# Performance work log

Hardware: AMD Instinct MI355X
Metric: run time of the kernel (lower is better)

The kernel has to match this reference:

```python
import jax, jax.numpy as jnp
import numpy as np

B, L, D = 2, 2048, 1024
H = 16          # num_heads == num_key_value_heads
FD = 16         # feature_dim (q/k head dim)
HD = D // H     # head_dim = 64 (v head dim)
EPS = 1e-5


def setup_inputs() -> dict:
    key = jax.random.key(0)
    k0, k1, k2, k3, k4 = jax.random.split(key, 5)
    scale = 0.02
    return {
        "hidden_states": jax.random.normal(k0, (B, L, D), jnp.float32),
        "Wq": jax.random.normal(k1, (D, H * FD), jnp.float32) * scale,
        "Wk": jax.random.normal(k2, (D, H * FD), jnp.float32) * scale,
        "Wv": jax.random.normal(k3, (D, H * HD), jnp.float32) * scale,
        "Wo": jax.random.normal(k4, (H * HD, D), jnp.float32) * scale,
    }


def reference(hidden_states, Wq, Wk, Wv, Wo):
    # projections (bias-free), split heads: b l (h d) -> b h l d
    q = (hidden_states @ Wq).reshape(B, L, H, FD).transpose(0, 2, 1, 3)
    k = (hidden_states @ Wk).reshape(B, L, H, FD).transpose(0, 2, 1, 3)
    v = (hidden_states @ Wv).reshape(B, L, H, HD).transpose(0, 2, 1, 3)

    # parallel_rebased: squared-dot-product kernel attention, causal,
    # row-normalized by the kernel sum (use_scale=True, use_normalize=True)
    qk_scale = FD ** -0.5
    s = jnp.einsum('bhqd,bhkd->bhqk', q * qk_scale, k)
    s = s * s  # quadratic feature map: (q.k)^2
    causal = jnp.tril(jnp.ones((L, L), dtype=bool))
    s = jnp.where(causal, s, 0.0)
    z = jnp.sum(s, axis=-1)  # [B,H,L]
    o = jnp.einsum('bhqk,bhkd->bhqd', s, v) / (z[..., None] + EPS)

    # merge heads: b h l d -> b l (h d), output projection
    o = o.transpose(0, 2, 1, 3).reshape(B, L, H * HD)
    return o @ Wo
```

## Files before the change

### kernel.cpp

```cpp
#include <hip/hip_runtime.h>
#include <hip/hip_bf16.h>

#define BB 2
#define LL 2048
#define DD 1024
#define HH 16
#define FD 16
#define HD 64
#define EPS 1e-5f
#define RQKV 1536
#define NFIX 4

typedef __attribute__((ext_vector_type(4))) float f32x4;
typedef __attribute__((ext_vector_type(8))) _Float16 f16x8;
typedef __attribute__((ext_vector_type(4))) _Float16 f16x4;

__global__ __launch_bounds__(256) void prep(
    const float* __restrict__ Wq, const float* __restrict__ Wk,
    const float* __restrict__ Wv, const float* __restrict__ Wo,
    const float* __restrict__ hs, _Float16* __restrict__ WqkvT,
    _Float16* __restrict__ WoT, float* __restrict__ QKVe,
    _Float16* __restrict__ HS16) {
  __shared__ __attribute__((aligned(16))) char smem[40960];
  const int bx = blockIdx.x;
  const int tid = threadIdx.x;

  if (bx >= 2608) {
    int idx = ((bx - 2608) * 256 + tid) * 16;
#pragma unroll
    for (int half = 0; half < 2; half++) {
      float4 a = *(const float4*)(hs + idx + half * 8);
      float4 b = *(const float4*)(hs + idx + half * 8 + 4);
      f16x8 p = {(_Float16)a.x, (_Float16)a.y, (_Float16)a.z, (_Float16)a.w,
                 (_Float16)b.x, (_Float16)b.y, (_Float16)b.z, (_Float16)b.w};
      *(f16x8*)(HS16 + idx + half * 8) = p;
    }
    return;
  }

  if (bx < 2560) {
    _Float16(*s)[40] = (_Float16(*)[40])smem;
    const float* src;
    _Float16* dst;
    int n0, ncol, drow, k0;
    if (bx < 1536) {
      int ct = bx % 48, kt = bx / 48;
      if (ct < 8) { src = Wq; n0 = ct * 32; ncol = 256; drow = n0; }
      else if (ct < 16) { src = Wk; n0 = (ct - 8) * 32; ncol = 256; drow = 256 + n0; }
      else { src = Wv; n0 = (ct - 16) * 32; ncol = 1024; drow = 512 + n0; }
      k0 = kt * 32;
      dst = WqkvT;
    } else {
      int i2 = bx - 1536;
      n0 = (i2 & 31) * 32; k0 = (i2 >> 5) * 32;
      src = Wo; ncol = DD; drow = n0; dst = WoT;
    }
    {
      int r = tid >> 3, c = (tid & 7) * 4;
      float4 v = *(const float4*)(src + (size_t)(k0 + r) * ncol + n0 + c);
      f16x4 p = {(_Float16)v.x, (_Float16)v.y, (_Float16)v.z, (_Float16)v.w};
      *(f16x4*)&s[r][c] = p;
    }
    __syncthreads();
    {
      int n = tid >> 3, kk = (tid & 7) * 4;
      f16x4 o = {s[kk + 0][n], s[kk + 1][n], s[kk + 2][n], s[kk + 3][n]};
      *(f16x4*)(dst + (size_t)(drow + n) * DD + k0 + kk) = o;
    }
    return;
  }

  float(*sHS)[DD] = (float(*)[DD])smem;
  float(*part)[8][32] = (float(*)[8][32])(smem + 32768);
  const int kg = tid >> 5, c = tid & 31;
  const int c0 = (bx - 2560) * 32;

  for (int i = tid; i < 8 * (DD / 4); i += 256) {
    int e = i / (DD / 4), col4 = (i % (DD / 4)) * 4;
    int b = e >> 2, r = e & 3;
    *(float4*)&sHS[e][col4] =
        *(const float4*)(hs + (size_t)(b * LL + r) * DD + col4);
  }
  __syncthreads();

  const float* W;
  int col, ncol;
  if (c0 < 256) { W = Wq; col = c0 + c; ncol = 256; }
  else if (c0 < 512) { W = Wk; col = (c0 - 256) + c; ncol = 256; }
  else { W = Wv; col = (c0 - 512) + c; ncol = 1024; }

  float acc[8] = {};
  const int d0 = kg * 128;
#pragma unroll 4
  for (int d = d0; d < d0 + 128; d++) {
    float wv = W[(size_t)d * ncol + col];
#pragma unroll
    for (int e = 0; e < 8; e++) acc[e] += sHS[e][d] * wv;
  }
#pragma unroll
  for (int e = 0; e < 8; e++) part[kg][e][c] = acc[e];
  __syncthreads();

  {
    int e = tid >> 5;
    float t = 0.f;
#pragma unroll
    for (int g = 0; g < 8; g++) t += part[g][e][c];
    QKVe[(size_t)e * RQKV + c0 + c] = t;
  }
}

template <typename OutT>
__global__ __launch_bounds__(256) void gemm_f16(
    const _Float16* __restrict__ A, const _Float16* __restrict__ Bt,
    OutT* __restrict__ C, int M, int N, int K) {
  __shared__ __attribute__((aligned(16))) _Float16 sA[128 * 64];
  __shared__ __attribute__((aligned(16))) _Float16 sB[64 * 64];
  const int tid = threadIdx.x;
  const int m0 = blockIdx.y * 128, n0 = blockIdx.x * 64;
  const int w = tid >> 6, lane = tid & 63, quad = lane >> 4, l16 = lane & 15;
  const int wm = (w >> 1) * 64, wn = (w & 1) * 32;

  const int sr = tid >> 1, p = tid & 1;
  const int brow = (tid & 127) >> 1;
  const _Float16* Ag = A + (size_t)(m0 + sr) * K + p * 32;
  const _Float16* Bg = Bt + (size_t)(n0 + brow) * K + p * 32;
  _Float16* sAw = &sA[sr * 64];
  _Float16* sBw = &sB[brow * 64];
  const int aswz = sr & 7, bswz = brow & 7;

  f32x4 acc[4][2];
#pragma unroll
  for (int i = 0; i < 4; i++)
#pragma unroll
    for (int j = 0; j < 2; j++) acc[i][j] = (f32x4){0.f, 0.f, 0.f, 0.f};

  f16x8 ar[4], br[4];
  auto LOAD = [&](int k0) {
#pragma unroll
    for (int i = 0; i < 4; i++) ar[i] = *(const f16x8*)(Ag + k0 + i * 8);
    if (tid < 128) {
#pragma unroll
      for (int i = 0; i < 4; i++) br[i] = *(const f16x8*)(Bg + k0 + i * 8);
    }
  };
  LOAD(0);

  for (int k0 = 0; k0 < K; k0 += 64) {
    __syncthreads();
#pragma unroll
    for (int i = 0; i < 4; i++)
      *(f16x8*)(sAw + (((4 * p + i) ^ aswz) * 8)) = ar[i];
    if (tid < 128) {
#pragma unroll
      for (int i = 0; i < 4; i++)
        *(f16x8*)(sBw + (((4 * p + i) ^ bswz) * 8)) = br[i];
    }
    __syncthreads();
    if (k0 + 64 < K) LOAD(k0 + 64);

#pragma unroll
    for (int s = 0; s < 2; s++) {
      f16x8 af[4], bf[2];
#pragma unroll
      for (int i = 0; i < 4; i++) {
        int row = wm + i * 16 + l16;
        int col = ((s * 4 + quad) ^ (row & 7)) * 8;
        af[i] = *(const f16x8*)&sA[row * 64 + col];
      }
#pragma unroll
      for (int j = 0; j < 2; j++) {
        int row = wn + j * 16 + l16;
        int col = ((s * 4 + quad) ^ (row & 7)) * 8;
        bf[j] = *(const f16x8*)&sB[row * 64 + col];
      }
#pragma unroll
      for (int i = 0; i < 4; i++)
#pragma unroll
        for (int j = 0; j < 2; j++)
          acc[i][j] = __builtin_amdgcn_mfma_f32_16x16x32_f16(af[i], bf[j], acc[i][j], 0, 0, 0);
    }
  }

#pragma unroll
  for (int i = 0; i < 4; i++)
#pragma unroll
    for (int j = 0; j < 2; j++)
#pragma unroll
      for (int r = 0; r < 4; r++) {
        const int row = m0 + wm + i * 16 + quad * 4 + r;
        const int col = n0 + wn + j * 16 + l16;
        C[(size_t)row * N + col] = (OutT)acc[i][j][r];
      }
}

#define SK5 24
#define SV5 136
#define SS5 88

__global__ __launch_bounds__(256, 4) void attn_mfma5(
    const _Float16* __restrict__ QKV, _Float16* __restrict__ O) {
  __shared__ __attribute__((aligned(16))) _Float16 sK[128 * SK5];
  __shared__ __attribute__((aligned(16))) _Float16 sVt[80 * SV5];
  __shared__ __attribute__((aligned(16))) _Float16 sS2[4 * 16 * SS5];

  const int bh = blockIdx.x;
  const int b = bh >> 4, h = bh & 15;
  const int qt = 31 - blockIdx.y;
  const int tid = threadIdx.x;
  const int w = tid >> 6;
  const int lane = tid & 63;
  const int quad = lane >> 4;
  const int l16 = lane & 15;
  const int gq = qt * 64 + w * 16;

  f16x8 qfrag = {};
  if (quad < 2) {
    qfrag = *(const f16x8*)(QKV +
        (size_t)(b * LL + gq + l16) * RQKV + h * FD + quad * 8);
    const _Float16 RT2 = (_Float16)1.41421356f;
#pragma unroll
    for (int i = 0; i < 8; i++) qfrag[i] = qfrag[i] * RT2;
  }

  for (int t = tid; t < 16 * SV5; t += 256) {
    int r = t / SV5, c = t % SV5;
    sVt[64 * SV5 + t] = (_Float16)((r == 0 && c < 128) ? 1.0f : 0.0f);
  }
  __syncthreads();
  const f16x8 zf0 = *(const f16x8*)&sVt[(64 + l16) * SV5 + quad * 8];
  const f16x8 zf1 = *(const f16x8*)&sVt[(64 + l16) * SV5 + 32 + quad * 8];

  f32x4 oacc[4];
  f32x4 zacc = (f32x4){0.f, 0.f, 0.f, 0.f};
#pragma unroll
  for (int nt = 0; nt < 4; nt++) oacc[nt] = (f32x4){0.f, 0.f, 0.f, 0.f};

  _Float16* sS2w = sS2 + w * 16 * SS5;

  const int nst = qt + 1;
  const int nkt = (nst + 1) >> 1;

  const int krow = tid >> 1, kcol = (tid & 1) * 8;
  f16x8 kreg;
  f16x8 vreg0, vreg1, vreg2, vreg3;
  auto LOAD = [&](int kt) {
    kreg = *(const f16x8*)(QKV +
        (size_t)(b * LL + kt * 128 + krow) * RQKV + 256 + h * FD + kcol);
    const _Float16* vp = QKV +
        (size_t)(b * LL + kt * 128 + lane) * RQKV + 512 + h * HD + w * 16;
    vreg0 = *(const f16x8*)vp;
    vreg1 = *(const f16x8*)(vp + 8);
    vp += (size_t)64 * RQKV;
    vreg2 = *(const f16x8*)vp;
    vreg3 = *(const f16x8*)(vp + 8);
  };
  LOAD(0);

  for (int kt = 0; kt < nkt; kt++) {
    __syncthreads();
    *(f16x8*)&sK[krow * SK5 + kcol] = kreg;
#pragma unroll
    for (int t = 0; t < 8; t++) sVt[(w * 16 + t) * SV5 + lane] = vreg0[t];
#pragma unroll
    for (int t = 0; t < 8; t++) sVt[(w * 16 + 8 + t) * SV5 + lane] = vreg1[t];
#pragma unroll
    for (int t = 0; t < 8; t++) sVt[(w * 16 + t) * SV5 + 64 + lane] = vreg2[t];
#pragma unroll
    for (int t = 0; t < 8; t++) sVt[(w * 16 + 8 + t) * SV5 + 64 + lane] = vreg3[t];
    __syncthreads();
    if (kt + 1 < nkt) LOAD(kt + 1);

#pragma unroll
    for (int hf = 0; hf < 2; hf++) {
      const int st = 2 * kt + hf;
      if (st >= nst) break;
      const int k0 = st * 64;
      const bool mask = (st == qt);

      f16x8 kf[4];
#pragma unroll
      for (int nt = 0; nt < 4; nt++) {
        f16x8 f = {};
        if (quad < 2)
          f = *(const f16x8*)&sK[(hf * 64 + nt * 16 + l16) * SK5 + quad * 8];
        kf[nt] = f;
      }

#pragma unroll
      for (int nt = 0; nt < 4; nt++) {
        f32x4 s = __builtin_amdgcn_mfma_f32_16x16x32_f16(
            qfrag, kf[nt], (f32x4){0.f, 0.f, 0.f, 0.f}, 0, 0, 0);
        const int gk = k0 + nt * 16 + l16;
#pragma unroll
        for (int r = 0; r < 4; r++) {
          float sv = s[r] * s[r];
          if (mask) sv = (gk <= gq + quad * 4 + r) ? sv : 0.0f;
          sS2w[(quad * 4 + r) * SS5 + nt * 16 + l16] = (_Float16)sv;
        }
      }
      __asm__ volatile("s_waitcnt lgkmcnt(0)" ::: "memory");

      f16x8 af0 = *(const f16x8*)&sS2w[l16 * SS5 + quad * 8];
      f16x8 af1 = *(const f16x8*)&sS2w[l16 * SS5 + 32 + quad * 8];

#pragma unroll
      for (int nt = 0; nt < 4; nt++) {
        f16x8 vf0 = *(const f16x8*)&sVt[(nt * 16 + l16) * SV5 + hf * 64 + quad * 8];
        f16x8 vf1 = *(const f16x8*)&sVt[(nt * 16 + l16) * SV5 + hf * 64 + 32 + quad * 8];
        oacc[nt] = __builtin_amdgcn_mfma_f32_16x16x32_f16(af0, vf0, oacc[nt], 0, 0, 0);
        oacc[nt] = __builtin_amdgcn_mfma_f32_16x16x32_f16(af1, vf1, oacc[nt], 0, 0, 0);
      }
      zacc = __builtin_amdgcn_mfma_f32_16x16x32_f16(af0, zf0, zacc, 0, 0, 0);
      zacc = __builtin_amdgcn_mfma_f32_16x16x32_f16(af1, zf1, zacc, 0, 0, 0);
    }
  }

  {
    float rz[4];
#pragma unroll
    for (int r = 0; r < 4; r++) {
      float zz = __shfl(zacc[r], lane & 48);
      rz[r] = 1.0f / (zz + 32.0f * EPS);
    }
#pragma unroll
    for (int nt = 0; nt < 4; nt++)
#pragma unroll
      for (int r = 0; r < 4; r++) {
        const int gqr = gq + quad * 4 + r;
        O[(size_t)(b * LL + gqr) * (HH * HD) + h * HD + nt * 16 + l16] =
            (_Float16)(oacc[nt][r] * rz[r]);
      }
  }
}

__global__ __launch_bounds__(256) void fix_final(
    const float* __restrict__ QKVe, _Float16* __restrict__ Oatt) {
  const int b = blockIdx.x >> 4, h = blockIdx.x & 15;
  const int tid = threadIdx.x;
  const int p = tid >> 6, d = tid & 63;

  float num = 0.f, z = 0.f;
  const float* qrow = QKVe + (size_t)(b * 4 + p) * RQKV + h * FD;
  for (int j = 0; j <= p; j++) {
    const float* krow = QKVe + (size_t)(b * 4 + j) * RQKV + 256 + h * FD;
    float s = 0.f;
#pragma unroll
    for (int f = 0; f < FD; f++) s += qrow[f] * krow[f];
    s *= 0.25f;
    s = s * s;
    z += s;
    num += s * QKVe[(size_t)(b * 4 + j) * RQKV + 512 + h * HD + d];
  }
  Oatt[(size_t)(b * LL + p) * (HH * HD) + h * HD + d] =
      (_Float16)(num / (z + EPS));
}

extern "C" void kernel_launch(void* const* d_in, const int* in_sizes, int n_in,
                              void* d_out, int out_size, void* d_ws, size_t ws_size,
                              hipStream_t stream) {
  const float* hs = (const float*)d_in[0];
  const float* Wq = (const float*)d_in[1];
  const float* Wk = (const float*)d_in[2];
  const float* Wv = (const float*)d_in[3];
  const float* Wo = (const float*)d_in[4];
  float* out = (float*)d_out;

  char* ws = (char*)d_ws;
  _Float16* WqkvT = (_Float16*)ws;
  _Float16* WoT   = (_Float16*)(ws + (3ull << 20));
  _Float16* HS16  = (_Float16*)(ws + (5ull << 20));
  _Float16* QKV   = (_Float16*)(ws + (13ull << 20));
  _Float16* Oatt  = (_Float16*)(ws + (25ull << 20));
  float*    QKVe  = (float*)(ws + (33ull << 20));

  const int M = BB * LL;

  prep<<<dim3(3632), 256, 0, stream>>>(Wq, Wk, Wv, Wo, hs, WqkvT, WoT, QKVe, HS16);

  gemm_f16<_Float16><<<dim3(RQKV / 64, M / 128), 256, 0, stream>>>(
      HS16, WqkvT, QKV, M, RQKV, DD);

  attn_mfma5<<<dim3(BB * HH, LL / 64), 256, 0, stream>>>(QKV, Oatt);

  fix_final<<<dim3(BB * HH), 256, 0, stream>>>(QKVe, Oatt);

  gemm_f16<float><<<dim3(DD / 64, M / 128), 256, 0, stream>>>(
      Oatt, WoT, out, M, DD, DD);
}
```

Before: 172.9 us.

## Keep squared scores in registers via transposed MFMA and permuted V layout

Computes the score tile as K·Qᵀ so each lane's accumulator lanes already match the A-operand layout of the next MFMA. The squared, masked scores are packed into f16 registers directly instead of round-tripping through a per-wave shared-memory buffer. To make this work, the V transpose in shared memory is stored with a permuted key-column index that matches the new score register ordering. Removing the scratch buffer frees LDS, and the launch-bounds occupancy hint rises from 4 to 5 blocks, at the cost of a more intricate lane-permutation invariant.

```diff
diff --git a/kernel.cpp b/kernel.cpp
--- a/kernel.cpp
+++ b/kernel.cpp
@@ -14,6 +14,7 @@
 typedef __attribute__((ext_vector_type(4))) float f32x4;
 typedef __attribute__((ext_vector_type(8))) _Float16 f16x8;
 typedef __attribute__((ext_vector_type(4))) _Float16 f16x4;
+typedef __attribute__((ext_vector_type(4))) unsigned int u32x4;
 
 __global__ __launch_bounds__(256) void prep(
     const float* __restrict__ Wq, const float* __restrict__ Wk,
@@ -194,15 +195,19 @@
       }
 }
 
+__device__ __forceinline__ unsigned pack_f16x2(float a, float b) {
+  unsigned short ua = __builtin_bit_cast(unsigned short, (_Float16)a);
+  unsigned short ub = __builtin_bit_cast(unsigned short, (_Float16)b);
+  return (unsigned)ua | ((unsigned)ub << 16);
+}
+
 #define SK5 24
 #define SV5 136
-#define SS5 88
-
-__global__ __launch_bounds__(256, 4) void attn_mfma5(
+
+__global__ __launch_bounds__(256, 5) void attn_mfma7(
     const _Float16* __restrict__ QKV, _Float16* __restrict__ O) {
   __shared__ __attribute__((aligned(16))) _Float16 sK[128 * SK5];
   __shared__ __attribute__((aligned(16))) _Float16 sVt[80 * SV5];
-  __shared__ __attribute__((aligned(16))) _Float16 sS2[4 * 16 * SS5];
 
   const int bh = blockIdx.x;
   const int b = bh >> 4, h = bh & 15;
@@ -214,6 +219,8 @@
   const int l16 = lane & 15;
   const int gq = qt * 64 + w * 16;
 
+  const int pc = (lane & 32) | ((lane & 12) << 1) | ((lane & 16) >> 2) | (lane & 3);
+
   f16x8 qfrag = {};
   if (quad < 2) {
     qfrag = *(const f16x8*)(QKV +
@@ -235,8 +242,6 @@
   f32x4 zacc = (f32x4){0.f, 0.f, 0.f, 0.f};
 #pragma unroll
   for (int nt = 0; nt < 4; nt++) oacc[nt] = (f32x4){0.f, 0.f, 0.f, 0.f};
-
-  _Float16* sS2w = sS2 + w * 16 * SS5;
 
   const int nst = qt + 1;
   const int nkt = (nst + 1) >> 1;
@@ -261,13 +266,13 @@
     __syncthreads();
     *(f16x8*)&sK[krow * SK5 + kcol] = kreg;
 #pragma unroll
-    for (int t = 0; t < 8; t++) sVt[(w * 16 + t) * SV5 + lane] = vreg0[t];
-#pragma unroll
-    for (int t = 0; t < 8; t++) sVt[(w * 16 + 8 + t) * SV5 + lane] = vreg1[t];
-#pragma unroll
-    for (int t = 0; t < 8; t++) sVt[(w * 16 + t) * SV5 + 64 + lane] = vreg2[t];
-#pragma unroll
-    for (int t = 0; t < 8; t++) sVt[(w * 16 + 8 + t) * SV5 + 64 + lane] = vreg3[t];
+    for (int t = 0; t < 8; t++) sVt[(w * 16 + t) * SV5 + pc] = vreg0[t];
+#pragma unroll
+    for (int t = 0; t < 8; t++) sVt[(w * 16 + 8 + t) * SV5 + pc] = vreg1[t];
+#pragma unroll
+    for (int t = 0; t < 8; t++) sVt[(w * 16 + t) * SV5 + 64 + pc] = vreg2[t];
+#pragma unroll
+    for (int t = 0; t < 8; t++) sVt[(w * 16 + 8 + t) * SV5 + 64 + pc] = vreg3[t];
     __syncthreads();
     if (kt + 1 < nkt) LOAD(kt + 1);
 
@@ -287,22 +292,29 @@
         kf[nt] = f;
       }
 
+      unsigned wp[4][2];
 #pragma unroll
       for (int nt = 0; nt < 4; nt++) {
         f32x4 s = __builtin_amdgcn_mfma_f32_16x16x32_f16(
-            qfrag, kf[nt], (f32x4){0.f, 0.f, 0.f, 0.f}, 0, 0, 0);
-        const int gk = k0 + nt * 16 + l16;
-#pragma unroll
-        for (int r = 0; r < 4; r++) {
-          float sv = s[r] * s[r];
-          if (mask) sv = (gk <= gq + quad * 4 + r) ? sv : 0.0f;
-          sS2w[(quad * 4 + r) * SS5 + nt * 16 + l16] = (_Float16)sv;
+            kf[nt], qfrag, (f32x4){0.f, 0.f, 0.f, 0.f}, 0, 0, 0);
+        float s0 = s[0] * s[0], s1 = s[1] * s[1];
+        float s2 = s[2] * s[2], s3 = s[3] * s[3];
+        if (mask) {
+          const int gkb = k0 + nt * 16 + quad * 4;
+          const int qg = gq + l16;
+          if (gkb + 0 > qg) s0 = 0.f;
+          if (gkb + 1 > qg) s1 = 0.f;
+          if (gkb + 2 > qg) s2 = 0.f;
+          if (gkb + 3 > qg) s3 = 0.f;
         }
-      }
-      __asm__ volatile("s_waitcnt lgkmcnt(0)" ::: "memory");
-
-      f16x8 af0 = *(const f16x8*)&sS2w[l16 * SS5 + quad * 8];
-      f16x8 af1 = *(const f16x8*)&sS2w[l16 * SS5 + 32 + quad * 8];
+        wp[nt][0] = pack_f16x2(s0, s1);
+        wp[nt][1] = pack_f16x2(s2, s3);
+      }
+
+      u32x4 u0 = {wp[0][0], wp[0][1], wp[1][0], wp[1][1]};
+      u32x4 u1 = {wp[2][0], wp[2][1], wp[3][0], wp[3][1]};
+      f16x8 af0 = __builtin_bit_cast(f16x8, u0);
+      f16x8 af1 = __builtin_bit_cast(f16x8, u1);
 
 #pragma unroll
       for (int nt = 0; nt < 4; nt++) {
@@ -381,7 +393,7 @@
   gemm_f16<_Float16><<<dim3(RQKV / 64, M / 128), 256, 0, stream>>>(
       HS16, WqkvT, QKV, M, RQKV, DD);
 
-  attn_mfma5<<<dim3(BB * HH, LL / 64), 256, 0, stream>>>(QKV, Oatt);
+  attn_mfma7<<<dim3(BB * HH, LL / 64), 256, 0, stream>>>(QKV, Oatt);
 
   fix_final<<<dim3(BB * HH), 256, 0, stream>>>(QKVe, Oatt);
 
```

Result: faster. 165.7 us (median of 2 runs) (-4.2%).
